# Kernel tuning notes

Hardware: AMD Instinct MI355X
Metric: run time of the kernel (lower is better)

## Reference

```python
import jax, jax.numpy as jnp
import numpy as np

B = 1024
N_NODES = 30
E_PER = 82
IN_F = 128
HID = 256
HEADS = (3, 2, 1)
N_EH = 41


def _lin(k, fi, fo):
    s = 1.0 / np.sqrt(fi)
    kw, kb = jax.random.split(k)
    W = jax.random.uniform(kw, (fi, fo), jnp.float32, -s, s)
    b = jax.random.uniform(kb, (fo,), jnp.float32, -s, s)
    return W, b


def setup_inputs() -> dict:
    key = jax.random.key(0)
    ks = list(jax.random.split(key, 32))
    rng = np.random.default_rng(0)
    # base 30-node graph with E_PER directed edges, no self-loops
    src = rng.integers(0, N_NODES, E_PER)
    dst = (src + rng.integers(1, N_NODES, E_PER)) % N_NODES
    base = np.stack([src, dst])  # [2, E_PER]
    offs = (np.arange(B) * N_NODES)[None, None, :]  # [1,1,B]
    ei = (base[:, :, None] + offs).transpose(0, 2, 1).reshape(2, -1)  # [2, B*E_PER]
    e_h = rng.choice(E_PER, N_EH, replace=False)
    d = {}
    d["x"] = jax.random.normal(ks[0], (B * N_NODES, IN_F), jnp.float32)
    d["edge_index"] = jnp.asarray(ei, dtype=jnp.int32)
    d["e_h_pairs"] = jnp.asarray(base[:, e_h].T, dtype=jnp.int32)  # [N_EH, 2]
    d["Wp"], d["bp"] = _lin(ks[1], IN_F, HID)
    i = 2
    for l, H in enumerate(HEADS):
        d[f"ln_g{l}"] = jnp.ones((HID,), jnp.float32)
        d[f"ln_b{l}"] = jnp.zeros((HID,), jnp.float32)
        d[f"Wl{l}"], d[f"bl{l}"] = _lin(ks[i], HID, H * HID); i += 1
        d[f"Wr{l}"], d[f"br{l}"] = _lin(ks[i], HID, H * HID); i += 1
        d[f"att{l}"] = jax.random.normal(ks[i], (H, HID), jnp.float32) * 0.1; i += 1
        d[f"bias{l}"] = jnp.zeros((HID,), jnp.float32)
    dims = [2 * HID, 256, 128, 128, 1]
    for j in range(4):
        d[f"Wm{j}"], d[f"bm{j}"] = _lin(ks[i], dims[j], dims[j + 1]); i += 1
    return d


def _layer_norm(h, g, b):
    mu = jnp.mean(h, -1, keepdims=True)
    var = jnp.mean((h - mu) ** 2, -1, keepdims=True)
    return (h - mu) * jax.lax.rsqrt(var + 1e-5) * g + b


def _gatv2(h, src, dst, n, Wl, bl, Wr, br, att, bias):
    # PyG GATv2Conv, concat=False (mean over heads), self-loops already in src/dst
    H, C = att.shape
    xl = (h @ Wl + bl).reshape(-1, H, C)  # source transform
    xr = (h @ Wr + br).reshape(-1, H, C)  # target transform
    xj = xl[src]                          # [E,H,C]
    e = jax.nn.leaky_relu(xj + xr[dst], 0.2)
    logits = jnp.einsum('ehc,hc->eh', e, att)  # [E,H]
    m = jax.lax.stop_gradient(jax.ops.segment_max(logits, dst, num_segments=n))
    ex = jnp.exp(logits - m[dst])
    denom = jax.ops.segment_sum(ex, dst, num_segments=n)
    alpha = ex / denom[dst]               # softmax over incoming edges of dst
    out = jax.ops.segment_sum(xj * alpha[..., None], dst, num_segments=n)  # [N,H,C]
    return jnp.mean(out, 1) + bias


def reference(x, edge_index, e_h_pairs, Wp, bp,
              ln_g0, ln_b0, Wl0, bl0, Wr0, br0, att0, bias0,
              ln_g1, ln_b1, Wl1, bl1, Wr1, br1, att1, bias1,
              ln_g2, ln_b2, Wl2, bl2, Wr2, br2, att2, bias2,
              Wm0, bm0, Wm1, bm1, Wm2, bm2, Wm3, bm3):
    n = x.shape[0]
    loops = jnp.arange(n, dtype=edge_index.dtype)
    src = jnp.concatenate([edge_index[0], loops])
    dst = jnp.concatenate([edge_index[1], loops])
    lrelu = lambda v: jax.nn.leaky_relu(v, 0.01)
    h = x @ Wp + bp
    layers = [(ln_g0, ln_b0, Wl0, bl0, Wr0, br0, att0, bias0),
              (ln_g1, ln_b1, Wl1, bl1, Wr1, br1, att1, bias1),
              (ln_g2, ln_b2, Wl2, bl2, Wr2, br2, att2, bias2)]
    for (g, b, Wl, bl, Wr, br, att, bias) in layers:
        hn = _layer_norm(h, g, b)
        hc = _gatv2(hn, src, dst, n, Wl, bl, Wr, br, att, bias)
        h = lrelu(hc) + h  # dropout is identity in eval
    hb = h.reshape(-1, N_NODES, HID)  # [B, 30, 256]
    ef = jnp.concatenate([hb[:, e_h_pairs[:, 0], :], hb[:, e_h_pairs[:, 1], :]], -1)
    o = ef.reshape(-1, 2 * HID)
    o = lrelu(o @ Wm0 + bm0)
    o = lrelu(o @ Wm1 + bm1)
    o = lrelu(o @ Wm2 + bm2)
    o = o @ Wm3 + bm3
    return o.reshape(-1)
```

## Files before the change

kernel.cpp:

```cpp
#include <hip/hip_runtime.h>
#include <hip/hip_bf16.h>
#include <math.h>

#define N_NODES 30
#define E_BASE  82
#define E_TOT   112
#define B_GRAPH 1024
#define HID     256
#define NTOT    (B_GRAPH * N_NODES)
#define MAXIN   32
#define N_EH    41
#define M_MLP   (B_GRAPH * N_EH)

#define META_SRC  0
#define META_DST  E_TOT
#define META_CNT  (2 * E_TOT)
#define META_LIST 256
#define META_INTS 1216

typedef __attribute__((ext_vector_type(8))) short bf16x8;
typedef __attribute__((ext_vector_type(4))) short bf16x4;
typedef __attribute__((ext_vector_type(4))) float f32x4;
#define AS3 __attribute__((address_space(3)))
#define AS1 __attribute__((address_space(1)))

__device__ __forceinline__ void gload_lds16(const void* g, void* l) {
  __builtin_amdgcn_global_load_lds((const AS1 void*)g, (AS3 void*)l, 16, 0, 0);
}

__device__ __forceinline__ float b2f(short s) {
  union { unsigned u; float f; } x;
  x.u = ((unsigned)(unsigned short)s) << 16;
  return x.f;
}

struct WtJob { const float* in; int K, N, tstart, ooff; };
struct WtArgs { WtJob j[10]; };

__global__ __launch_bounds__(256)
void transpose_weights(WtArgs args, __hip_bfloat16* __restrict__ out,
                       const int* __restrict__ ei, int* __restrict__ meta) {
  int b = blockIdx.x;
  if (b == 976) {
    __shared__ int cnt[N_NODES];
    int tid = threadIdx.x;
    if (tid < N_NODES) cnt[tid] = 0;
    __syncthreads();
    if (tid < E_TOT) {
      int s, d;
      if (tid < E_BASE) { s = ei[tid]; d = ei[B_GRAPH * E_BASE + tid]; }
      else              { s = tid - E_BASE; d = s; }
      meta[META_SRC + tid] = s;
      meta[META_DST + tid] = d;
      int pos = atomicAdd(&cnt[d], 1);
      if (pos < MAXIN) meta[META_LIST + d * MAXIN + pos] = tid;
    }
    __syncthreads();
    if (tid < N_NODES) meta[META_CNT + tid] = cnt[tid];
    return;
  }
  int ji = 0;
  #pragma unroll
  for (int i = 1; i < 10; i++) if (b >= args.j[i].tstart) ji = i;
  WtJob jb = args.j[ji];
  int t = b - jb.tstart;
  int ntn = jb.N >> 5;
  int tk = t / ntn, tn = t - tk * ntn;
  int k0 = tk * 32, n0 = tn * 32;
  __shared__ float s[32][33];
  int tx = threadIdx.x & 31, ty = threadIdx.x >> 5;
  #pragma unroll
  for (int p = 0; p < 4; p++)
    s[ty + p * 8][tx] = jb.in[(size_t)(k0 + ty + p * 8) * jb.N + n0 + tx];
  __syncthreads();
  __hip_bfloat16* o = out + jb.ooff;
  #pragma unroll
  for (int p = 0; p < 4; p++) {
    int n = ty + p * 8;
    o[(size_t)(n0 + n) * jb.K + k0 + tx] = __float2bfloat16(s[tx][n]);
  }
}

template<int ACT, int OUTBF>
__global__ __launch_bounds__(256)
void gemm_mfma(const __hip_bfloat16* __restrict__ A, const __hip_bfloat16* __restrict__ Bt,
               const float* __restrict__ bias, const float* __restrict__ bias2,
               void* __restrict__ Cv, int M, int K, int N, int N1)
{
  __shared__ __hip_bfloat16 sA[128 * 32];
  __shared__ __hip_bfloat16 sB[128 * 32];
  const int tid = threadIdx.x;
  const int lane = tid & 63;
  const int wave = tid >> 6;
  const int wx = wave & 1, wy = wave >> 1;
  const int bm = blockIdx.x, bn = blockIdx.y;
  const int mrow = lane & 15, quad = lane >> 4;

  const int r0 = tid >> 2, kc0 = (tid & 3) * 8;
  const __hip_bfloat16* Ag0 = A + (size_t)(bm * 128 + r0) * K + kc0;
  const __hip_bfloat16* Ag1 = A + (size_t)(bm * 128 + r0 + 64) * K + kc0;
  const __hip_bfloat16* Bg0 = Bt + (size_t)(bn * 128 + r0) * K + kc0;
  const __hip_bfloat16* Bg1 = Bt + (size_t)(bn * 128 + r0 + 64) * K + kc0;

  f32x4 acc[4][4];
  #pragma unroll
  for (int i = 0; i < 4; i++)
    #pragma unroll
    for (int j = 0; j < 4; j++)
      acc[i][j] = (f32x4){0.f, 0.f, 0.f, 0.f};

  for (int kt = 0; kt < K; kt += 32) {
    __syncthreads();
    gload_lds16(Ag0 + kt, &sA[tid * 8]);
    gload_lds16(Ag1 + kt, &sA[2048 + tid * 8]);
    gload_lds16(Bg0 + kt, &sB[tid * 8]);
    gload_lds16(Bg1 + kt, &sB[2048 + tid * 8]);
    __syncthreads();

    bf16x8 af[4], bfr[4];
    #pragma unroll
    for (int i = 0; i < 4; i++) {
      af[i]  = *(const bf16x8*)&sA[(wy * 64 + i * 16 + mrow) * 32 + quad * 8];
      bfr[i] = *(const bf16x8*)&sB[(wx * 64 + i * 16 + mrow) * 32 + quad * 8];
    }
    #pragma unroll
    for (int i = 0; i < 4; i++)
      #pragma unroll
      for (int j = 0; j < 4; j++)
        acc[i][j] = __builtin_amdgcn_mfma_f32_16x16x32_bf16(af[i], bfr[j], acc[i][j], 0, 0, 0);
  }

  #pragma unroll
  for (int i = 0; i < 4; i++) {
    #pragma unroll
    for (int r = 0; r < 4; r++) {
      size_t row = (size_t)bm * 128 + wy * 64 + i * 16 + quad * 4 + r;
      #pragma unroll
      for (int j = 0; j < 4; j++) {
        int col = bn * 128 + wx * 64 + j * 16 + mrow;
        float bc = (col < N1) ? bias[col] : bias2[col - N1];
        float v = acc[i][j][r] + bc;
        if (ACT) v = v > 0.f ? v : 0.01f * v;
        if (OUTBF) ((__hip_bfloat16*)Cv)[row * N + col] = __float2bfloat16(v);
        else       ((float*)Cv)[row * N + col] = v;
      }
    }
  }
}

template<int ACT, int OUTBF>
__global__ __launch_bounds__(256)
void gemm_mfma_f32a(const float* __restrict__ A, const __hip_bfloat16* __restrict__ Bt,
                    const float* __restrict__ bias, void* __restrict__ Cv,
                    int M, int K, int N)
{
  __shared__ __hip_bfloat16 sA[128 * 32];
  __shared__ __hip_bfloat16 sB[128 * 32];
  const int tid = threadIdx.x;
  const int lane = tid & 63;
  const int wave = tid >> 6;
  const int wx = wave & 1, wy = wave >> 1;
  const int bm = blockIdx.x, bn = blockIdx.y;
  const int mrow = lane & 15, quad = lane >> 4;

  const int r0 = tid >> 2, kc0 = (tid & 3) * 8;
  const float* Ag0 = A + (size_t)(bm * 128 + r0) * K + kc0;
  const float* Ag1 = A + (size_t)(bm * 128 + r0 + 64) * K + kc0;
  const __hip_bfloat16* Bg0 = Bt + (size_t)(bn * 128 + r0) * K + kc0;
  const __hip_bfloat16* Bg1 = Bt + (size_t)(bn * 128 + r0 + 64) * K + kc0;

  f32x4 acc[4][4];
  #pragma unroll
  for (int i = 0; i < 4; i++)
    #pragma unroll
    for (int j = 0; j < 4; j++)
      acc[i][j] = (f32x4){0.f, 0.f, 0.f, 0.f};

  for (int kt = 0; kt < K; kt += 32) {
    float4 a00 = *(const float4*)(Ag0 + kt);
    float4 a01 = *(const float4*)(Ag0 + kt + 4);
    float4 a10 = *(const float4*)(Ag1 + kt);
    float4 a11 = *(const float4*)(Ag1 + kt + 4);
    __syncthreads();
    {
      __hip_bfloat16 t[8];
      t[0] = __float2bfloat16(a00.x); t[1] = __float2bfloat16(a00.y);
      t[2] = __float2bfloat16(a00.z); t[3] = __float2bfloat16(a00.w);
      t[4] = __float2bfloat16(a01.x); t[5] = __float2bfloat16(a01.y);
      t[6] = __float2bfloat16(a01.z); t[7] = __float2bfloat16(a01.w);
      *(bf16x8*)&sA[tid * 8] = *(bf16x8*)t;
      t[0] = __float2bfloat16(a10.x); t[1] = __float2bfloat16(a10.y);
      t[2] = __float2bfloat16(a10.z); t[3] = __float2bfloat16(a10.w);
      t[4] = __float2bfloat16(a11.x); t[5] = __float2bfloat16(a11.y);
      t[6] = __float2bfloat16(a11.z); t[7] = __float2bfloat16(a11.w);
      *(bf16x8*)&sA[2048 + tid * 8] = *(bf16x8*)t;
    }
    gload_lds16(Bg0 + kt, &sB[tid * 8]);
    gload_lds16(Bg1 + kt, &sB[2048 + tid * 8]);
    __syncthreads();

    bf16x8 af[4], bfr[4];
    #pragma unroll
    for (int i = 0; i < 4; i++) {
      af[i]  = *(const bf16x8*)&sA[(wy * 64 + i * 16 + mrow) * 32 + quad * 8];
      bfr[i] = *(const bf16x8*)&sB[(wx * 64 + i * 16 + mrow) * 32 + quad * 8];
    }
    #pragma unroll
    for (int i = 0; i < 4; i++)
      #pragma unroll
      for (int j = 0; j < 4; j++)
        acc[i][j] = __builtin_amdgcn_mfma_f32_16x16x32_bf16(af[i], bfr[j], acc[i][j], 0, 0, 0);
  }

  #pragma unroll
  for (int i = 0; i < 4; i++) {
    #pragma unroll
    for (int r = 0; r < 4; r++) {
      size_t row = (size_t)bm * 128 + wy * 64 + i * 16 + quad * 4 + r;
      #pragma unroll
      for (int j = 0; j < 4; j++) {
        int col = bn * 128 + wx * 64 + j * 16 + mrow;
        float v = acc[i][j][r] + bias[col];
        if (ACT) v = v > 0.f ? v : 0.01f * v;
        if (OUTBF) ((__hip_bfloat16*)Cv)[row * N + col] = __float2bfloat16(v);
        else       ((float*)Cv)[row * N + col] = v;
      }
    }
  }
}

__global__ __launch_bounds__(256)
void gemm_mfma_pair(const float* __restrict__ h, const int* __restrict__ pairs,
                    const __hip_bfloat16* __restrict__ Bt, const float* __restrict__ bias,
                    __hip_bfloat16* __restrict__ C, int N)
{
  const int K = 512;
  __shared__ __hip_bfloat16 sA[128 * 32];
  __shared__ __hip_bfloat16 sB[128 * 32];
  const int tid = threadIdx.x;
  const int lane = tid & 63;
  const int wave = tid >> 6;
  const int wx = wave & 1, wy = wave >> 1;
  const int bm = blockIdx.x, bn = blockIdx.y;
  const int mrow = lane & 15, quad = lane >> 4;

  const float* pu[2]; const float* pv[2]; int sub[2];
  #pragma unroll
  for (int cI = 0; cI < 2; cI++) {
    int c = tid + cI * 256;
    int r0 = c >> 2; sub[cI] = (c & 3) * 8;
    int R = bm * 128 + r0;
    int b = R / N_EH, p = R - b * N_EH;
    int u = pairs[p * 2], v = pairs[p * 2 + 1];
    pu[cI] = h + ((size_t)b * N_NODES + u) * HID;
    pv[cI] = h + ((size_t)b * N_NODES + v) * HID;
  }

  const int r0 = tid >> 2, kc0 = (tid & 3) * 8;
  const __hip_bfloat16* Bg0 = Bt + (size_t)(bn * 128 + r0) * K + kc0;
  const __hip_bfloat16* Bg1 = Bt + (size_t)(bn * 128 + r0 + 64) * K + kc0;

  f32x4 acc[4][4];
  #pragma unroll
  for (int i = 0; i < 4; i++)
    #pragma unroll
    for (int j = 0; j < 4; j++)
      acc[i][j] = (f32x4){0.f, 0.f, 0.f, 0.f};

  for (int kt = 0; kt < K; kt += 32) {
    float4 av[2][2];
    #pragma unroll
    for (int cI = 0; cI < 2; cI++) {
      const float* src = (kt < 256 ? pu[cI] + kt : pv[cI] + kt - 256) + sub[cI];
      av[cI][0] = *(const float4*)src;
      av[cI][1] = *(const float4*)(src + 4);
    }
    __syncthreads();
    #pragma unroll
    for (int cI = 0; cI < 2; cI++) {
      __hip_bfloat16 t[8];
      t[0] = __float2bfloat16(av[cI][0].x); t[1] = __float2bfloat16(av[cI][0].y);
      t[2] = __float2bfloat16(av[cI][0].z); t[3] = __float2bfloat16(av[cI][0].w);
      t[4] = __float2bfloat16(av[cI][1].x); t[5] = __float2bfloat16(av[cI][1].y);
      t[6] = __float2bfloat16(av[cI][1].z); t[7] = __float2bfloat16(av[cI][1].w);
      *(bf16x8*)&sA[(tid + cI * 256) * 8] = *(bf16x8*)t;
    }
    gload_lds16(Bg0 + kt, &sB[tid * 8]);
    gload_lds16(Bg1 + kt, &sB[2048 + tid * 8]);
    __syncthreads();

    bf16x8 af[4], bfr[4];
    #pragma unroll
    for (int i = 0; i < 4; i++) {
      af[i]  = *(const bf16x8*)&sA[(wy * 64 + i * 16 + mrow) * 32 + quad * 8];
      bfr[i] = *(const bf16x8*)&sB[(wx * 64 + i * 16 + mrow) * 32 + quad * 8];
    }
    #pragma unroll
    for (int i = 0; i < 4; i++)
      #pragma unroll
      for (int j = 0; j < 4; j++)
        acc[i][j] = __builtin_amdgcn_mfma_f32_16x16x32_bf16(af[i], bfr[j], acc[i][j], 0, 0, 0);
  }

  #pragma unroll
  for (int i = 0; i < 4; i++) {
    #pragma unroll
    for (int r = 0; r < 4; r++) {
      size_t row = (size_t)bm * 128 + wy * 64 + i * 16 + quad * 4 + r;
      #pragma unroll
      for (int j = 0; j < 4; j++) {
        int col = bn * 128 + wx * 64 + j * 16 + mrow;
        float v = acc[i][j][r] + bias[col];
        v = v > 0.f ? v : 0.01f * v;
        C[row * N + col] = __float2bfloat16(v);
      }
    }
  }
}

#define O2P 136
__global__ __launch_bounds__(256)
void mlp_tail(const __hip_bfloat16* __restrict__ o1, const __hip_bfloat16* __restrict__ W1t,
              const float* __restrict__ b1, const __hip_bfloat16* __restrict__ W2t,
              const float* __restrict__ b2, const float* __restrict__ w3,
              const float* __restrict__ b3, float* __restrict__ out)
{
  __shared__ __hip_bfloat16 sA[128 * 32];
  __shared__ __hip_bfloat16 sB[128 * 32];
  __shared__ __hip_bfloat16 sO2[128 * O2P];
  __shared__ float spart[2][128];
  const int tid = threadIdx.x;
  const int lane = tid & 63;
  const int wave = tid >> 6;
  const int wx = wave & 1, wy = wave >> 1;
  const int bm = blockIdx.x;
  const int mrow = lane & 15, quad = lane >> 4;
  const int r0 = tid >> 2, kc0 = (tid & 3) * 8;

  const __hip_bfloat16* Ag0 = o1 + (size_t)(bm * 128 + r0) * 256 + kc0;
  const __hip_bfloat16* Ag1 = o1 + (size_t)(bm * 128 + r0 + 64) * 256 + kc0;
  const __hip_bfloat16* Bg0 = W1t + (size_t)r0 * 256 + kc0;
  const __hip_bfloat16* Bg1 = W1t + (size_t)(r0 + 64) * 256 + kc0;

  f32x4 acc[4][4];
  #pragma unroll
  for (int i = 0; i < 4; i++)
    #pragma unroll
    for (int j = 0; j < 4; j++)
      acc[i][j] = (f32x4){0.f, 0.f, 0.f, 0.f};

  for (int kt = 0; kt < 256; kt += 32) {
    __syncthreads();
    gload_lds16(Ag0 + kt, &sA[tid * 8]);
    gload_lds16(Ag1 + kt, &sA[2048 + tid * 8]);
    gload_lds16(Bg0 + kt, &sB[tid * 8]);
    gload_lds16(Bg1 + kt, &sB[2048 + tid * 8]);
    __syncthreads();

    bf16x8 af[4], bfr[4];
    #pragma unroll
    for (int i = 0; i < 4; i++) {
      af[i]  = *(const bf16x8*)&sA[(wy * 64 + i * 16 + mrow) * 32 + quad * 8];
      bfr[i] = *(const bf16x8*)&sB[(wx * 64 + i * 16 + mrow) * 32 + quad * 8];
    }
    #pragma unroll
    for (int i = 0; i < 4; i++)
      #pragma unroll
      for (int j = 0; j < 4; j++)
        acc[i][j] = __builtin_amdgcn_mfma_f32_16x16x32_bf16(af[i], bfr[j], acc[i][j], 0, 0, 0);
  }

  __syncthreads();
  #pragma unroll
  for (int i = 0; i < 4; i++) {
    #pragma unroll
    for (int r = 0; r < 4; r++) {
      int row = wy * 64 + i * 16 + quad * 4 + r;
      #pragma unroll
      for (int j = 0; j < 4; j++) {
        int col = wx * 64 + j * 16 + mrow;
        float v = acc[i][j][r] + b1[col];
        v = v > 0.f ? v : 0.01f * v;
        sO2[row * O2P + col] = __float2bfloat16(v);
      }
    }
  }

  f32x4 acc2[4][4];
  #pragma unroll
  for (int i = 0; i < 4; i++)
    #pragma unroll
    for (int j = 0; j < 4; j++)
      acc2[i][j] = (f32x4){0.f, 0.f, 0.f, 0.f};

  for (int kt = 0; kt < 128; kt += 32) {
    __syncthreads();
    gload_lds16(W2t + (size_t)r0 * 128 + kt + kc0, &sB[tid * 8]);
    gload_lds16(W2t + (size_t)(r0 + 64) * 128 + kt + kc0, &sB[2048 + tid * 8]);
    __syncthreads();

    bf16x8 af[4], bfr[4];
    #pragma unroll
    for (int i = 0; i < 4; i++) {
      af[i]  = *(const bf16x8*)&sO2[(wy * 64 + i * 16 + mrow) * O2P + kt + quad * 8];
      bfr[i] = *(const bf16x8*)&sB[(wx * 64 + i * 16 + mrow) * 32 + quad * 8];
    }
    #pragma unroll
    for (int i = 0; i < 4; i++)
      #pragma unroll
      for (int j = 0; j < 4; j++)
        acc2[i][j] = __builtin_amdgcn_mfma_f32_16x16x32_bf16(af[i], bfr[j], acc2[i][j], 0, 0, 0);
  }

  float w3v[4], b2v[4];
  #pragma unroll
  for (int j = 0; j < 4; j++) {
    int col = wx * 64 + j * 16 + mrow;
    w3v[j] = w3[col];
    b2v[j] = b2[col];
  }
  #pragma unroll
  for (int i = 0; i < 4; i++) {
    #pragma unroll
    for (int r = 0; r < 4; r++) {
      float s = 0.f;
      #pragma unroll
      for (int j = 0; j < 4; j++) {
        float v = acc2[i][j][r] + b2v[j];
        v = v > 0.f ? v : 0.01f * v;
        s += v * w3v[j];
      }
      #pragma unroll
      for (int off = 8; off; off >>= 1) s += __shfl_xor(s, off);
      if (mrow == 0) {
        int row = wy * 64 + i * 16 + quad * 4 + r;
        spart[wx][row] = s;
      }
    }
  }
  __syncthreads();
  if (tid < 128)
    out[(size_t)bm * 128 + tid] = spart[0][tid] + spart[1][tid] + b3[0];
}

__global__ __launch_bounds__(256)
void layernorm(const float* __restrict__ h, const float* __restrict__ g,
               const float* __restrict__ b, __hip_bfloat16* __restrict__ hn)
{
  const int wv = threadIdx.x >> 6, lane = threadIdx.x & 63;
  const size_t row = (size_t)blockIdx.x * 4 + wv;
  const float* hr = h + row * HID;
  float v[4];
  float sum = 0.f;
  #pragma unroll
  for (int j = 0; j < 4; j++) { v[j] = hr[lane + 64 * j]; sum += v[j]; }
  #pragma unroll
  for (int off = 32; off; off >>= 1) sum += __shfl_xor(sum, off);
  float mu = sum * (1.f / 256.f);
  float vs = 0.f;
  #pragma unroll
  for (int j = 0; j < 4; j++) { float d = v[j] - mu; vs += d * d; }
  #pragma unroll
  for (int off = 32; off; off >>= 1) vs += __shfl_xor(vs, off);
  float rs = rsqrtf(vs * (1.f / 256.f) + 1e-5f);
  __hip_bfloat16* outr = hn + row * HID;
  #pragma unroll
  for (int j = 0; j < 4; j++) {
    int c = lane + 64 * j;
    outr[c] = __float2bfloat16((v[j] - mu) * rs * g[c] + b[c]);
  }
}

__global__ __launch_bounds__(256)
void gat_alpha(const __hip_bfloat16* __restrict__ xcat,
               const float* __restrict__ att, float* __restrict__ alphaG,
               const int* __restrict__ meta, int H)
{
  __shared__ __hip_bfloat16 sxl[N_NODES * HID];
  __shared__ __hip_bfloat16 sxr[N_NODES * HID];
  __shared__ float slog[E_TOT];
  __shared__ float smax[N_NODES];
  __shared__ float sden[N_NODES];
  __shared__ int ssrc[E_TOT], sdst[E_TOT], scnt[N_NODES], slist[N_NODES * MAXIN];

  const int tid = threadIdx.x;
  const int g = blockIdx.x, hh = blockIdx.y;
  const size_t nodebase = (size_t)g * N_NODES;
  const int S = 2 * H * HID;

  {
    int i = tid;
    #pragma unroll
    for (int p = 0; p < 4; p++, i += 256) {
      if (i < N_NODES * HID / 8) {
        int node = i >> 5, c = (i & 31) * 8;
        const __hip_bfloat16* row = &xcat[(nodebase + node) * S + c];
        gload_lds16(row + hh * HID, &sxl[(size_t)i * 8]);
        gload_lds16(row + (H + hh) * HID, &sxr[(size_t)i * 8]);
      }
    }
  }

  if (tid < E_TOT) { ssrc[tid] = meta[META_SRC + tid]; sdst[tid] = meta[META_DST + tid]; }
  if (tid < N_NODES) { scnt[tid] = meta[META_CNT + tid]; sden[tid] = 0.f; }
  for (int i = tid; i < N_NODES * MAXIN; i += 256) slist[i] = meta[META_LIST + i];

  const int wv = tid >> 6, l32 = tid & 31, esub = (tid >> 5) & 1;
  const int c0 = l32 * 8;
  float attr[8];
  #pragma unroll
  for (int j = 0; j < 8; j++) attr[j] = att[hh * HID + c0 + j];
  __syncthreads();

  #pragma unroll
  for (int pass = 0; pass < 14; pass++) {
    int e = pass * 8 + wv * 2 + esub;
    bf16x8 a = *(const bf16x8*)&sxl[ssrc[e] * HID + c0];
    bf16x8 b = *(const bf16x8*)&sxr[sdst[e] * HID + c0];
    float sum = 0.f;
    #pragma unroll
    for (int j = 0; j < 8; j++) {
      float v = b2f(a[j]) + b2f(b[j]);
      v = v > 0.f ? v : 0.2f * v;
      sum += v * attr[j];
    }
    #pragma unroll
    for (int off = 16; off; off >>= 1) sum += __shfl_xor(sum, off);
    if (l32 == 0) slog[e] = sum;
  }
  __syncthreads();

  if (tid < N_NODES) {
    int cnt = scnt[tid];
    const int* lst = &slist[tid * MAXIN];
    float m = -1e30f;
    for (int i = 0; i < cnt; i++) m = fmaxf(m, slog[lst[i]]);
    smax[tid] = m;
  }
  __syncthreads();
  if (tid < E_TOT) {
    float ex = expf(slog[tid] - smax[sdst[tid]]);
    slog[tid] = ex;
    atomicAdd(&sden[sdst[tid]], ex);
  }
  __syncthreads();
  if (tid < E_TOT)
    alphaG[((size_t)g * H + hh) * E_TOT + tid] = slog[tid] / sden[sdst[tid]];
}

template<int DO_LN>
__global__ __launch_bounds__(256, 4)
void gat_agg(const __hip_bfloat16* __restrict__ xcat, const float* __restrict__ alphaG,
             const float* __restrict__ bias, float* __restrict__ h,
             const float* __restrict__ lnG, const float* __restrict__ lnB,
             __hip_bfloat16* __restrict__ hn, const int* __restrict__ meta, int H)
{
  __shared__ __hip_bfloat16 sxl[2][N_NODES * HID];
  __shared__ float salpha[2][E_TOT];
  __shared__ int ssrc[E_TOT], scnt[N_NODES], slist[N_NODES * MAXIN];

  const int tid = threadIdx.x;
  const int g = blockIdx.x;
  const size_t nodebase = (size_t)g * N_NODES;
  const int S = 2 * H * HID;
  const int c4 = tid & 63;
  const int ng = tid >> 6;

  if (tid < E_TOT) ssrc[tid] = meta[META_SRC + tid];
  if (tid < N_NODES) scnt[tid] = meta[META_CNT + tid];
  for (int i = tid; i < N_NODES * MAXIN; i += 256) slist[i] = meta[META_LIST + i];

  float4 hres[8];
  #pragma unroll
  for (int ki = 0; ki < 8; ki++) {
    int k = ng + ki * 4;
    if (k < N_NODES) hres[ki] = *(const float4*)&h[(nodebase + k) * HID + c4 * 4];
  }

  {
    int i = tid;
    #pragma unroll
    for (int p = 0; p < 4; p++, i += 256) {
      if (i < N_NODES * HID / 8) {
        int node = i >> 5, c = (i & 31) * 8;
        gload_lds16(&xcat[(nodebase + node) * S + 0 * HID + c], &sxl[0][(size_t)i * 8]);
      }
    }
    if (tid < E_TOT) salpha[0][tid] = alphaG[((size_t)g * H + 0) * E_TOT + tid];
  }

  float acc[8][4];
  #pragma unroll
  for (int ki = 0; ki < 8; ki++)
    #pragma unroll
    for (int j = 0; j < 4; j++) acc[ki][j] = 0.f;

  for (int hh = 0; hh < H; hh++) {
    const int buf = hh & 1;
    __syncthreads();
    if (hh + 1 < H) {
      const int nb = buf ^ 1;
      int i = tid;
      #pragma unroll
      for (int p = 0; p < 4; p++, i += 256) {
        if (i < N_NODES * HID / 8) {
          int node = i >> 5, c = (i & 31) * 8;
          gload_lds16(&xcat[(nodebase + node) * S + (hh + 1) * HID + c], &sxl[nb][(size_t)i * 8]);
        }
      }
      if (tid < E_TOT) salpha[nb][tid] = alphaG[((size_t)g * H + hh + 1) * E_TOT + tid];
    }
    #pragma unroll
    for (int ki = 0; ki < 8; ki++) {
      int k = ng + ki * 4;
      if (k < N_NODES) {
        int cnt = scnt[k];
        const int* lst = &slist[k * MAXIN];
        for (int i = 0; i < cnt; i++) {
          int e = lst[i];
          float al = salpha[buf][e];
          bf16x4 v = *(const bf16x4*)&sxl[buf][ssrc[e] * HID + c4 * 4];
          acc[ki][0] += al * b2f(v[0]);
          acc[ki][1] += al * b2f(v[1]);
          acc[ki][2] += al * b2f(v[2]);
          acc[ki][3] += al * b2f(v[3]);
        }
      }
    }
  }

  const float invH = 1.f / (float)H;
  const float4 bs = *(const float4*)&bias[c4 * 4];
  float4 gv, bv;
  if (DO_LN) {
    gv = *(const float4*)&lnG[c4 * 4];
    bv = *(const float4*)&lnB[c4 * 4];
  }
  #pragma unroll
  for (int ki = 0; ki < 8; ki++) {
    int k = ng + ki * 4;
    if (k < N_NODES) {
      float o0 = acc[ki][0] * invH + bs.x; o0 = o0 > 0.f ? o0 : 0.01f * o0; o0 += hres[ki].x;
      float o1 = acc[ki][1] * invH + bs.y; o1 = o1 > 0.f ? o1 : 0.01f * o1; o1 += hres[ki].y;
      float o2 = acc[ki][2] * invH + bs.z; o2 = o2 > 0.f ? o2 : 0.01f * o2; o2 += hres[ki].z;
      float o3 = acc[ki][3] * invH + bs.w; o3 = o3 > 0.f ? o3 : 0.01f * o3; o3 += hres[ki].w;
      float4 o4 = {o0, o1, o2, o3};
      *(float4*)&h[(nodebase + k) * HID + c4 * 4] = o4;
      if (DO_LN) {
        float sum = o0 + o1 + o2 + o3;
        #pragma unroll
        for (int off = 32; off; off >>= 1) sum += __shfl_xor(sum, off);
        float mu = sum * (1.f / 256.f);
        float d0 = o0 - mu, d1 = o1 - mu, d2 = o2 - mu, d3 = o3 - mu;
        float vs = d0 * d0 + d1 * d1 + d2 * d2 + d3 * d3;
        #pragma unroll
        for (int off = 32; off; off >>= 1) vs += __shfl_xor(vs, off);
        float rs = rsqrtf(vs * (1.f / 256.f) + 1e-5f);
        __hip_bfloat16 t[4];
        t[0] = __float2bfloat16(d0 * rs * gv.x + bv.x);
        t[1] = __float2bfloat16(d1 * rs * gv.y + bv.y);
        t[2] = __float2bfloat16(d2 * rs * gv.z + bv.z);
        t[3] = __float2bfloat16(d3 * rs * gv.w + bv.w);
        *(bf16x4*)&hn[(nodebase + k) * HID + c4 * 4] = *(bf16x4*)t;
      }
    }
  }
}

extern "C" void kernel_launch(void* const* d_in, const int* in_sizes, int n_in,
                              void* d_out, int out_size, void* d_ws, size_t ws_size,
                              hipStream_t stream) {
  const float* x     = (const float*)d_in[0];
  const int*   ei    = (const int*)d_in[1];
  const int*   pairs = (const int*)d_in[2];
  const float* bp    = (const float*)d_in[4];
  const float *lng[3], *lnb[3], *bl[3], *br[3], *att[3], *bias[3];
  const float *WlF[3], *WrF[3];
  for (int l = 0; l < 3; l++) {
    int base = 5 + l * 8;
    lng[l]  = (const float*)d_in[base + 0];
    lnb[l]  = (const float*)d_in[base + 1];
    WlF[l]  = (const float*)d_in[base + 2];
    bl[l]   = (const float*)d_in[base + 3];
    WrF[l]  = (const float*)d_in[base + 4];
    br[l]   = (const float*)d_in[base + 5];
    att[l]  = (const float*)d_in[base + 6];
    bias[l] = (const float*)d_in[base + 7];
  }
  const float* WmF[4] = {(const float*)d_in[29], (const float*)d_in[31],
                         (const float*)d_in[33], (const float*)d_in[35]};
  const float* bm[4] = {(const float*)d_in[30], (const float*)d_in[32],
                        (const float*)d_in[34], (const float*)d_in[36]};

  float* ws  = (float*)d_ws;
  float* h   = ws;
  __hip_bfloat16* hnb = (__hip_bfloat16*)(ws + 7864320);
  __hip_bfloat16* xcat = (__hip_bfloat16*)(ws + 11796480);
  float* alphaG = ws + 35389440;
  __hip_bfloat16* wbuf = (__hip_bfloat16*)(ws + 35733504);
  int*   meta = (int*)(ws + 36233216);
  __hip_bfloat16* o1b = (__hip_bfloat16*)xcat;
  float* out = (float*)d_out;

  const int oWp = 0, oWl0 = 32768, oWr0 = 229376, oWl1 = 425984, oWr1 = 557056;
  const int oWl2 = 688128, oWr2 = 753664, oWm0 = 819200, oWm1 = 950272, oWm2 = 983040;

  WtArgs wa;
  wa.j[0] = {(const float*)d_in[3], 128, 256,   0, oWp };
  wa.j[1] = {WlF[0],              256, 768,  32, oWl0};
  wa.j[2] = {WrF[0],              256, 768, 224, oWr0};
  wa.j[3] = {WlF[1],              256, 512, 416, oWl1};
  wa.j[4] = {WrF[1],              256, 512, 544, oWr1};
  wa.j[5] = {WlF[2],              256, 256, 672, oWl2};
  wa.j[6] = {WrF[2],              256, 256, 736, oWr2};
  wa.j[7] = {WmF[0],              512, 256, 800, oWm0};
  wa.j[8] = {WmF[1],              256, 128, 928, oWm1};
  wa.j[9] = {WmF[2],              128, 128, 960, oWm2};
  transpose_weights<<<977, 256, 0, stream>>>(wa, wbuf, ei, meta);

  gemm_mfma_f32a<0, 0><<<dim3(NTOT / 128, 2), 256, 0, stream>>>(x, wbuf + oWp, bp, h,
                                                                NTOT, 128, 256);

  layernorm<<<NTOT / 4, 256, 0, stream>>>(h, lng[0], lnb[0], hnb);

  const int Hs[3] = {3, 2, 1};
  const int oWl[3] = {oWl0, oWl1, oWl2};
  for (int l = 0; l < 3; l++) {
    int N = 2 * Hs[l] * HID;
    gemm_mfma<0, 1><<<dim3(NTOT / 128, N / 128), 256, 0, stream>>>(
        hnb, wbuf + oWl[l], bl[l], br[l], xcat, NTOT, HID, N, N / 2);
    gat_alpha<<<dim3(B_GRAPH, Hs[l]), 256, 0, stream>>>(xcat, att[l], alphaG, meta, Hs[l]);
    if (l < 2)
      gat_agg<1><<<B_GRAPH, 256, 0, stream>>>(xcat, alphaG, bias[l], h,
                                              lng[l + 1], lnb[l + 1], hnb, meta, Hs[l]);
    else
      gat_agg<0><<<B_GRAPH, 256, 0, stream>>>(xcat, alphaG, bias[l], h,
                                              nullptr, nullptr, nullptr, meta, Hs[l]);
  }

  gemm_mfma_pair<<<dim3(M_MLP / 128, 2), 256, 0, stream>>>(h, pairs, wbuf + oWm0, bm[0], o1b, 256);
  mlp_tail<<<M_MLP / 128, 256, 0, stream>>>(o1b, wbuf + oWm1, bm[1], wbuf + oWm2, bm[2],
                                            WmF[3], bm[3], out);
}
```

Before: 443.6 us.

## Split GAT aggregation across channel halves and unfuse layernorm; deepen GEMM K-step

```diff
diff --git a/kernel.cpp b/kernel.cpp
--- a/kernel.cpp
+++ b/kernel.cpp
@@ -87,8 +87,8 @@
                const float* __restrict__ bias, const float* __restrict__ bias2,
                void* __restrict__ Cv, int M, int K, int N, int N1)
 {
-  __shared__ __hip_bfloat16 sA[128 * 32];
-  __shared__ __hip_bfloat16 sB[128 * 32];
+  __shared__ __hip_bfloat16 sA[2][128 * 32];
+  __shared__ __hip_bfloat16 sB[2][128 * 32];
   const int tid = threadIdx.x;
   const int lane = tid & 63;
   const int wave = tid >> 6;
@@ -109,25 +109,31 @@
     for (int j = 0; j < 4; j++)
       acc[i][j] = (f32x4){0.f, 0.f, 0.f, 0.f};
 
-  for (int kt = 0; kt < K; kt += 32) {
-    __syncthreads();
-    gload_lds16(Ag0 + kt, &sA[tid * 8]);
-    gload_lds16(Ag1 + kt, &sA[2048 + tid * 8]);
-    gload_lds16(Bg0 + kt, &sB[tid * 8]);
-    gload_lds16(Bg1 + kt, &sB[2048 + tid * 8]);
-    __syncthreads();
-
-    bf16x8 af[4], bfr[4];
-    #pragma unroll
-    for (int i = 0; i < 4; i++) {
-      af[i]  = *(const bf16x8*)&sA[(wy * 64 + i * 16 + mrow) * 32 + quad * 8];
-      bfr[i] = *(const bf16x8*)&sB[(wx * 64 + i * 16 + mrow) * 32 + quad * 8];
-    }
-    #pragma unroll
-    for (int i = 0; i < 4; i++)
-      #pragma unroll
-      for (int j = 0; j < 4; j++)
-        acc[i][j] = __builtin_amdgcn_mfma_f32_16x16x32_bf16(af[i], bfr[j], acc[i][j], 0, 0, 0);
+  for (int kt = 0; kt < K; kt += 64) {
+    __syncthreads();
+    #pragma unroll
+    for (int s = 0; s < 2; s++) {
+      gload_lds16(Ag0 + kt + s * 32, &sA[s][tid * 8]);
+      gload_lds16(Ag1 + kt + s * 32, &sA[s][2048 + tid * 8]);
+      gload_lds16(Bg0 + kt + s * 32, &sB[s][tid * 8]);
+      gload_lds16(Bg1 + kt + s * 32, &sB[s][2048 + tid * 8]);
+    }
+    __syncthreads();
+
+    #pragma unroll
+    for (int s = 0; s < 2; s++) {
+      bf16x8 af[4], bfr[4];
+      #pragma unroll
+      for (int i = 0; i < 4; i++) {
+        af[i]  = *(const bf16x8*)&sA[s][(wy * 64 + i * 16 + mrow) * 32 + quad * 8];
+        bfr[i] = *(const bf16x8*)&sB[s][(wx * 64 + i * 16 + mrow) * 32 + quad * 8];
+      }
+      #pragma unroll
+      for (int i = 0; i < 4; i++)
+        #pragma unroll
+        for (int j = 0; j < 4; j++)
+          acc[i][j] = __builtin_amdgcn_mfma_f32_16x16x32_bf16(af[i], bfr[j], acc[i][j], 0, 0, 0);
+    }
   }
 
   #pragma unroll
@@ -548,50 +554,50 @@
     alphaG[((size_t)g * H + hh) * E_TOT + tid] = slog[tid] / sden[sdst[tid]];
 }
 
-template<int DO_LN>
-__global__ __launch_bounds__(256, 4)
+__global__ __launch_bounds__(256, 8)
 void gat_agg(const __hip_bfloat16* __restrict__ xcat, const float* __restrict__ alphaG,
              const float* __restrict__ bias, float* __restrict__ h,
-             const float* __restrict__ lnG, const float* __restrict__ lnB,
-             __hip_bfloat16* __restrict__ hn, const int* __restrict__ meta, int H)
+             const int* __restrict__ meta, int H)
 {
-  __shared__ __hip_bfloat16 sxl[2][N_NODES * HID];
+  __shared__ __hip_bfloat16 sxl[2][N_NODES * 128];
   __shared__ float salpha[2][E_TOT];
   __shared__ int ssrc[E_TOT], scnt[N_NODES], slist[N_NODES * MAXIN];
 
   const int tid = threadIdx.x;
-  const int g = blockIdx.x;
+  const int g = blockIdx.x, hf = blockIdx.y;
   const size_t nodebase = (size_t)g * N_NODES;
   const int S = 2 * H * HID;
-  const int c4 = tid & 63;
-  const int ng = tid >> 6;
+  const int coff = hf * 128;
+  const int c4 = tid & 31;
+  const int ng = tid >> 5;
+  const int NCHK = N_NODES * 128 / 8;
 
   if (tid < E_TOT) ssrc[tid] = meta[META_SRC + tid];
   if (tid < N_NODES) scnt[tid] = meta[META_CNT + tid];
   for (int i = tid; i < N_NODES * MAXIN; i += 256) slist[i] = meta[META_LIST + i];
 
-  float4 hres[8];
-  #pragma unroll
-  for (int ki = 0; ki < 8; ki++) {
-    int k = ng + ki * 4;
-    if (k < N_NODES) hres[ki] = *(const float4*)&h[(nodebase + k) * HID + c4 * 4];
+  float4 hres[4];
+  #pragma unroll
+  for (int ki = 0; ki < 4; ki++) {
+    int k = ng + ki * 8;
+    if (k < N_NODES) hres[ki] = *(const float4*)&h[(nodebase + k) * HID + coff + c4 * 4];
   }
 
   {
     int i = tid;
     #pragma unroll
-    for (int p = 0; p < 4; p++, i += 256) {
-      if (i < N_NODES * HID / 8) {
-        int node = i >> 5, c = (i & 31) * 8;
-        gload_lds16(&xcat[(nodebase + node) * S + 0 * HID + c], &sxl[0][(size_t)i * 8]);
+    for (int p = 0; p < 2; p++, i += 256) {
+      if (i < NCHK) {
+        int node = i >> 4, c = (i & 15) * 8;
+        gload_lds16(&xcat[(nodebase + node) * S + 0 * HID + coff + c], &sxl[0][(size_t)i * 8]);
       }
     }
     if (tid < E_TOT) salpha[0][tid] = alphaG[((size_t)g * H + 0) * E_TOT + tid];
   }
 
-  float acc[8][4];
-  #pragma unroll
-  for (int ki = 0; ki < 8; ki++)
+  float acc[4][4];
+  #pragma unroll
+  for (int ki = 0; ki < 4; ki++)
     #pragma unroll
     for (int j = 0; j < 4; j++) acc[ki][j] = 0.f;
 
@@ -602,24 +608,25 @@
       const int nb = buf ^ 1;
       int i = tid;
       #pragma unroll
-      for (int p = 0; p < 4; p++, i += 256) {
-        if (i < N_NODES * HID / 8) {
-          int node = i >> 5, c = (i & 31) * 8;
-          gload_lds16(&xcat[(nodebase + node) * S + (hh + 1) * HID + c], &sxl[nb][(size_t)i * 8]);
+      for (int p = 0; p < 2; p++, i += 256) {
+        if (i < NCHK) {
+          int node = i >> 4, c = (i & 15) * 8;
+          gload_lds16(&xcat[(nodebase + node) * S + (hh + 1) * HID + coff + c],
+                      &sxl[nb][(size_t)i * 8]);
         }
       }
       if (tid < E_TOT) salpha[nb][tid] = alphaG[((size_t)g * H + hh + 1) * E_TOT + tid];
     }
     #pragma unroll
-    for (int ki = 0; ki < 8; ki++) {
-      int k = ng + ki * 4;
+    for (int ki = 0; ki < 4; ki++) {
+      int k = ng + ki * 8;
       if (k < N_NODES) {
         int cnt = scnt[k];
         const int* lst = &slist[k * MAXIN];
         for (int i = 0; i < cnt; i++) {
           int e = lst[i];
           float al = salpha[buf][e];
-          bf16x4 v = *(const bf16x4*)&sxl[buf][ssrc[e] * HID + c4 * 4];
+          bf16x4 v = *(const bf16x4*)&sxl[buf][ssrc[e] * 128 + c4 * 4];
           acc[ki][0] += al * b2f(v[0]);
           acc[ki][1] += al * b2f(v[1]);
           acc[ki][2] += al * b2f(v[2]);
@@ -630,39 +637,17 @@
   }
 
   const float invH = 1.f / (float)H;
-  const float4 bs = *(const float4*)&bias[c4 * 4];
-  float4 gv, bv;
-  if (DO_LN) {
-    gv = *(const float4*)&lnG[c4 * 4];
-    bv = *(const float4*)&lnB[c4 * 4];
-  }
-  #pragma unroll
-  for (int ki = 0; ki < 8; ki++) {
-    int k = ng + ki * 4;
+  const float4 bs = *(const float4*)&bias[coff + c4 * 4];
+  #pragma unroll
+  for (int ki = 0; ki < 4; ki++) {
+    int k = ng + ki * 8;
     if (k < N_NODES) {
       float o0 = acc[ki][0] * invH + bs.x; o0 = o0 > 0.f ? o0 : 0.01f * o0; o0 += hres[ki].x;
       float o1 = acc[ki][1] * invH + bs.y; o1 = o1 > 0.f ? o1 : 0.01f * o1; o1 += hres[ki].y;
       float o2 = acc[ki][2] * invH + bs.z; o2 = o2 > 0.f ? o2 : 0.01f * o2; o2 += hres[ki].z;
       float o3 = acc[ki][3] * invH + bs.w; o3 = o3 > 0.f ? o3 : 0.01f * o3; o3 += hres[ki].w;
       float4 o4 = {o0, o1, o2, o3};
-      *(float4*)&h[(nodebase + k) * HID + c4 * 4] = o4;
-      if (DO_LN) {
-        float sum = o0 + o1 + o2 + o3;
-        #pragma unroll
-        for (int off = 32; off; off >>= 1) sum += __shfl_xor(sum, off);
-        float mu = sum * (1.f / 256.f);
-        float d0 = o0 - mu, d1 = o1 - mu, d2 = o2 - mu, d3 = o3 - mu;
-        float vs = d0 * d0 + d1 * d1 + d2 * d2 + d3 * d3;
-        #pragma unroll
-        for (int off = 32; off; off >>= 1) vs += __shfl_xor(vs, off);
-        float rs = rsqrtf(vs * (1.f / 256.f) + 1e-5f);
-        __hip_bfloat16 t[4];
-        t[0] = __float2bfloat16(d0 * rs * gv.x + bv.x);
-        t[1] = __float2bfloat16(d1 * rs * gv.y + bv.y);
-        t[2] = __float2bfloat16(d2 * rs * gv.z + bv.z);
-        t[3] = __float2bfloat16(d3 * rs * gv.w + bv.w);
-        *(bf16x4*)&hn[(nodebase + k) * HID + c4 * 4] = *(bf16x4*)t;
-      }
+      *(float4*)&h[(nodebase + k) * HID + coff + c4 * 4] = o4;
     }
   }
 }
@@ -730,12 +715,9 @@
     gemm_mfma<0, 1><<<dim3(NTOT / 128, N / 128), 256, 0, stream>>>(
         hnb, wbuf + oWl[l], bl[l], br[l], xcat, NTOT, HID, N, N / 2);
     gat_alpha<<<dim3(B_GRAPH, Hs[l]), 256, 0, stream>>>(xcat, att[l], alphaG, meta, Hs[l]);
+    gat_agg<<<dim3(B_GRAPH, 2), 256, 0, stream>>>(xcat, alphaG, bias[l], h, meta, Hs[l]);
     if (l < 2)
-      gat_agg<1><<<B_GRAPH, 256, 0, stream>>>(xcat, alphaG, bias[l], h,
-                                              lng[l + 1], lnb[l + 1], hnb, meta, Hs[l]);
-    else
-      gat_agg<0><<<B_GRAPH, 256, 0, stream>>>(xcat, alphaG, bias[l], h,
-                                              nullptr, nullptr, nullptr, meta, Hs[l]);
+      layernorm<<<NTOT / 4, 256, 0, stream>>>(h, lng[l + 1], lnb[l + 1], hnb);
   }
 
   gemm_mfma_pair<<<dim3(M_MLP / 128, 2), 256, 0, stream>>>(h, pairs, wbuf + oWm0, bm[0], o1b, 256);
```

Result: no change. 451.9 us (+1.9%).
